# Kernel optimization log

Measured on AMD Instinct MI355X. Metric: run time of the kernel, lower is better.

The kernel has to match this reference:

```python
import jax, jax.numpy as jnp
import numpy as np

B, T, C, H = 2, 2048, 384, 6
HD = C // H
SINK_ITERS = 6  # MAX_ITER_SINK
EPS_LN = 1e-5


def layer_norm(x, w, b):
    mu = jnp.mean(x, axis=-1, keepdims=True)
    var = jnp.var(x, axis=-1, keepdims=True)
    return (x - mu) * jax.lax.rsqrt(var + EPS_LN) * w + b


def sinkhorn(c):
    # Log-domain Sinkhorn (sinkformers SinkhornDistance, eps=1, uniform 1/T marginals).
    # c: (B,H,T,T) row-softmaxed attention. C_cost=-c so M(C,u,v)= c + u_i + v_j.
    logT = jnp.log(jnp.asarray(T, c.dtype))
    u = jnp.zeros(c.shape[:-1], c.dtype)  # (B,H,T)
    v = jnp.zeros(c.shape[:-1], c.dtype)
    for i in range(SINK_ITERS):
        if i % 2 == 0:
            u = u - logT - jax.nn.logsumexp(c + u[..., :, None] + v[..., None, :], axis=-1)
        else:
            v = v - logT - jax.nn.logsumexp(c + u[..., :, None] + v[..., None, :], axis=-2)
            v = jax.lax.stop_gradient(v)  # torch code detaches v each odd iter
    return jnp.exp(c + u[..., :, None] + v[..., None, :])


def setup_inputs() -> dict:
    key = jax.random.key(0)
    ks = jax.random.split(key, 8)
    s = 0.02
    return {
        "x": jax.random.normal(ks[0], (B, T, C), jnp.float32),
        "t": jax.random.uniform(ks[1], (1,), jnp.float32),
        "ln1_w": jnp.ones((C + 1,), jnp.float32),
        "ln1_b": jnp.zeros((C + 1,), jnp.float32),
        "attn_w": (jax.random.normal(ks[2], (C + 1, 3 * C), jnp.float32) * s),  # torch W.T
        "attn_b": jnp.zeros((3 * C,), jnp.float32),
        "proj_w": (jax.random.normal(ks[3], (C, C), jnp.float32) * s),
        "proj_b": jnp.zeros((C,), jnp.float32),
        "ln2_w": jnp.ones((C + 1,), jnp.float32),
        "ln2_b": jnp.zeros((C + 1,), jnp.float32),
        "fc_w": (jax.random.normal(ks[4], (C + 1, 4 * C), jnp.float32) * s),
        "fc_b": jnp.zeros((4 * C,), jnp.float32),
        "fc2_w": (jax.random.normal(ks[5], (4 * C, C), jnp.float32) * s),
        "fc2_b": jnp.zeros((C,), jnp.float32),
    }


def add_time(h, t):
    b, tt, _ = h.shape
    tcol = jnp.broadcast_to(t.reshape(1, 1, 1).astype(h.dtype), (b, tt, 1))
    return jnp.concatenate([h, tcol], axis=-1)


def reference(x, t, ln1_w, ln1_b, attn_w, attn_b, proj_w, proj_b,
              ln2_w, ln2_b, fc_w, fc_b, fc2_w, fc2_b):
    # ---- attention sub-block ----
    xt = add_time(x, t)                       # (B,T,C+1)
    xn = layer_norm(xt, ln1_w, ln1_b)
    qkv = xn @ attn_w + attn_b                # (B,T,3C)
    q, k, vv = jnp.split(qkv, 3, axis=-1)
    q = q.reshape(B, T, H, HD).transpose(0, 2, 1, 3)   # (B,H,T,HD)
    k = k.reshape(B, T, H, HD).transpose(0, 2, 1, 3)
    vv = vv.reshape(B, T, H, HD).transpose(0, 2, 1, 3)
    att = jnp.einsum('bhqd,bhkd->bhqk', q, k) * (1.0 / np.sqrt(HD))
    causal = jnp.tril(jnp.ones((T, T), bool))
    att = jnp.where(causal, att, -jnp.inf)
    att = jax.nn.softmax(att, axis=-1)
    pi = sinkhorn(att) * T                    # sinked_att * last-dim size
    y = jnp.einsum('bhqk,bhkd->bhqd', pi, vv)
    y = y.transpose(0, 2, 1, 3).reshape(B, T, C)
    h = y @ proj_w + proj_b                   # (B,T,C)
    # ---- MLP sub-block ----
    ht = add_time(h, t)
    hn = layer_norm(ht, ln2_w, ln2_b)
    m = jax.nn.gelu(hn @ fc_w + fc_b, approximate=False)
    o = m @ fc2_w + fc2_b
    return o
```

## Files before the change

kernel.cpp:

```cpp
#include <hip/hip_runtime.h>
#include <hip/hip_fp16.h>
#include <math.h>

#define B 2
#define T 2048
#define C 384
#define H 6
#define HD 64
#define BHT (B*H*T)
#define LOGT 7.6246189861593985f

typedef __half half_t;
typedef _Float16 f16x8 __attribute__((ext_vector_type(8)));
typedef float f32x4 __attribute__((ext_vector_type(4)));

__device__ __forceinline__ float block_reduce_sum(float v) {
    __shared__ float sm[4];
    int lane = threadIdx.x & 63, wid = threadIdx.x >> 6;
#pragma unroll
    for (int o = 32; o > 0; o >>= 1) v += __shfl_down(v, o, 64);
    __syncthreads();
    if (lane == 0) sm[wid] = v;
    __syncthreads();
    return sm[0] + sm[1] + sm[2] + sm[3];
}

__device__ __forceinline__ float wave_allreduce_sum(float v) {
#pragma unroll
    for (int o = 1; o < 64; o <<= 1) v += __shfl_xor(v, o, 64);
    return v;
}

__global__ __launch_bounds__(256) void zerof_kernel(float* __restrict__ p) {
    p[(size_t)blockIdx.x * 256 + threadIdx.x] = 0.f;
}

__global__ __launch_bounds__(256) void addtime_ln_f16(
        const float* __restrict__ src, const float* __restrict__ tptr,
        const float* __restrict__ w, const float* __restrict__ bb,
        _Float16* __restrict__ dst, int KP) {
    const int n = C + 1;
    int row = blockIdx.x;
    const float* srow = src + (size_t)row * C;
    float tval = tptr[0];
    int i0 = threadIdx.x;
    int i1 = threadIdx.x + 256;
    float v0 = srow[i0];
    bool has1 = (i1 < n);
    float v1 = 0.f;
    if (has1) v1 = (i1 < C) ? srow[i1] : tval;
    float s  = block_reduce_sum(v0 + v1);
    float sq = block_reduce_sum(v0*v0 + v1*v1);
    float mean = s / n;
    float var  = sq / n - mean * mean;
    float rstd = rsqrtf(var + 1e-5f);
    _Float16* drow = dst + (size_t)row * KP;
    drow[i0] = (_Float16)((v0 - mean) * rstd * w[i0] + bb[i0]);
    if (has1) drow[i1] = (_Float16)((v1 - mean) * rstd * w[i1] + bb[i1]);
    else if (i1 < KP) drow[i1] = (_Float16)0.f;
}

__global__ __launch_bounds__(256) void convtrans_kernel(const float* __restrict__ W,
        _Float16* __restrict__ Wt, int K, int N, int KP) {
    __shared__ float tile[32][33];
    int k0 = blockIdx.x * 32, n0 = blockIdx.y * 32;
    int tx = threadIdx.x & 31, ty = threadIdx.x >> 5;
#pragma unroll
    for (int i = 0; i < 4; ++i) {
        int k = k0 + ty + i * 8, n = n0 + tx;
        tile[ty + i * 8][tx] = (k < K && n < N) ? W[(size_t)k * N + n] : 0.f;
    }
    __syncthreads();
#pragma unroll
    for (int i = 0; i < 4; ++i) {
        int n = n0 + ty + i * 8, k = k0 + tx;
        if (n < N && k < KP) Wt[(size_t)n * KP + k] = (_Float16)tile[tx][ty + i * 8];
    }
}

__device__ __forceinline__ f16x8 load8(const _Float16* p) { return *(const f16x8*)p; }
__device__ __forceinline__ f16x8 load8(const float* p) {
    float4 a = *(const float4*)p, b2 = *(const float4*)(p + 4);
    f16x8 r;
    r[0]=(_Float16)a.x; r[1]=(_Float16)a.y; r[2]=(_Float16)a.z; r[3]=(_Float16)a.w;
    r[4]=(_Float16)b2.x; r[5]=(_Float16)b2.y; r[6]=(_Float16)b2.z; r[7]=(_Float16)b2.w;
    return r;
}

template<int ACT, int QKV, typename AT, typename OUT_T>
__global__ __launch_bounds__(256) void mfma_gemm(
        const AT* __restrict__ A, const _Float16* __restrict__ Wt,
        const float* __restrict__ bias, OUT_T* __restrict__ out,
        int M, int N, int KP) {
    __shared__ __align__(16) _Float16 As[64][40];
    __shared__ __align__(16) _Float16 Bs[64][40];
    int tid = threadIdx.x;
    int lane = tid & 63, wave = tid >> 6;
    int wr = wave >> 1, wc = wave & 1;
    int m0 = blockIdx.y * 64, n0 = blockIdx.x * 64;
    int arow = tid >> 2, seg = tid & 3;
    int lrow = lane & 15, lseg = lane >> 4;
    f32x4 acc[2][2] = {};
    for (int k0 = 0; k0 < KP; k0 += 32) {
        __syncthreads();
        *(f16x8*)&As[arow][seg * 8] = load8(&A[(size_t)(m0 + arow) * KP + k0 + seg * 8]);
        *(f16x8*)&Bs[arow][seg * 8] = *(const f16x8*)&Wt[(size_t)(n0 + arow) * KP + k0 + seg * 8];
        __syncthreads();
        f16x8 af[2], bf[2];
#pragma unroll
        for (int i = 0; i < 2; ++i) af[i] = *(const f16x8*)&As[wr*32 + i*16 + lrow][lseg*8];
#pragma unroll
        for (int j = 0; j < 2; ++j) bf[j] = *(const f16x8*)&Bs[wc*32 + j*16 + lrow][lseg*8];
#pragma unroll
        for (int i = 0; i < 2; ++i)
#pragma unroll
            for (int j = 0; j < 2; ++j)
                acc[i][j] = __builtin_amdgcn_mfma_f32_16x16x32_f16(af[i], bf[j], acc[i][j], 0, 0, 0);
    }
    int lcol = lane & 15, lr4 = (lane >> 4) * 4;
#pragma unroll
    for (int i = 0; i < 2; ++i)
#pragma unroll
        for (int j = 0; j < 2; ++j) {
            int col = n0 + wc * 32 + j * 16 + lcol;
            float bv = bias[col];
#pragma unroll
            for (int r = 0; r < 4; ++r) {
                int row = m0 + wr * 32 + i * 16 + lr4 + r;
                float v = acc[i][j][r] + bv;
                if (ACT == 1) v = 0.5f * v * (1.f + erff(v * 0.70710678118654752f));
                if (QKV) {
                    int wq = col / C;
                    int rem = col - wq * C;
                    int hh = rem >> 6, dd = rem & 63;
                    int bb2 = row >> 11, tt = row & 2047;
                    out[(((size_t)wq * (B*H) + bb2 * H + hh) * T + tt) * 64 + dd] = (OUT_T)v;
                } else {
                    out[(size_t)row * N + col] = (OUT_T)v;
                }
            }
        }
}

__global__ __launch_bounds__(256) void qk_tileA(const _Float16* __restrict__ qh,
        const _Float16* __restrict__ kh, half_t* __restrict__ c_h) {
    int p = blockIdx.x, bh = blockIdx.y;
    int qt = (int)((sqrtf(8.f * (float)p + 1.f) - 1.f) * 0.5f);
    while ((qt + 1) * (qt + 2) / 2 <= p) ++qt;
    while (qt * (qt + 1) / 2 > p) --qt;
    int jt = p - qt * (qt + 1) / 2;
    int tid = threadIdx.x, lane = tid & 63, wave = tid >> 6;
    int wr = wave >> 1, wc = wave & 1;
    int lrow = lane & 15, lseg = lane >> 4;
    int orow = (lane >> 4) * 4, ocol = lane & 15;
    __shared__ __align__(16) _Float16 Qs[64][72];
    __shared__ __align__(16) _Float16 Ks[64][72];
    const _Float16* qb = qh + ((size_t)bh * T + qt * 64) * 64;
    const _Float16* kb = kh + ((size_t)bh * T + jt * 64) * 64;
#pragma unroll
    for (int k = 0; k < 2; ++k) {
        int cc = k * 256 + tid;
        int r = cc >> 3, sg = cc & 7;
        *(f16x8*)&Qs[r][sg*8] = *(const f16x8*)&qb[r*64 + sg*8];
        *(f16x8*)&Ks[r][sg*8] = *(const f16x8*)&kb[r*64 + sg*8];
    }
    __syncthreads();
    f32x4 acc[2][2] = {};
    f16x8 af[2], bf[2];
#pragma unroll
    for (int i = 0; i < 2; ++i) af[i] = *(const f16x8*)&Qs[wr*32+i*16+lrow][lseg*8];
#pragma unroll
    for (int j = 0; j < 2; ++j) bf[j] = *(const f16x8*)&Ks[wc*32+j*16+lrow][lseg*8];
#pragma unroll
    for (int i = 0; i < 2; ++i)
#pragma unroll
        for (int j = 0; j < 2; ++j)
            acc[i][j] = __builtin_amdgcn_mfma_f32_16x16x32_f16(af[i], bf[j], acc[i][j], 0,0,0);
#pragma unroll
    for (int i = 0; i < 2; ++i) af[i] = *(const f16x8*)&Qs[wr*32+i*16+lrow][32+lseg*8];
#pragma unroll
    for (int j = 0; j < 2; ++j) bf[j] = *(const f16x8*)&Ks[wc*32+j*16+lrow][32+lseg*8];
#pragma unroll
    for (int i = 0; i < 2; ++i)
#pragma unroll
        for (int j = 0; j < 2; ++j)
            acc[i][j] = __builtin_amdgcn_mfma_f32_16x16x32_f16(af[i], bf[j], acc[i][j], 0,0,0);
    __syncthreads();
    bool diag = (qt == jt);
#pragma unroll
    for (int i = 0; i < 2; ++i)
#pragma unroll
        for (int r = 0; r < 4; ++r) {
            int rl = wr*32 + i*16 + orow + r;
#pragma unroll
            for (int j = 0; j < 2; ++j) {
                int cl = wc*32 + j*16 + ocol;
                float s = acc[i][j][r] * 0.125f;
                float e = (diag && cl > rl) ? 0.f : __expf(s);
                Ks[rl][cl] = (_Float16)e;
            }
        }
    __syncthreads();
    half_t* cb = c_h + ((size_t)bh * T + qt * 64) * T + jt * 64;
#pragma unroll
    for (int k = 0; k < 2; ++k) {
        int cc = k * 256 + tid;
        int r = cc >> 3, sg = cc & 7;
        *(uint4*)&cb[(size_t)r * T + sg*8] = *(const uint4*)&Ks[r][sg*8];
    }
}

__global__ __launch_bounds__(256) void norm_q_u0(half_t* __restrict__ c_h,
        float* __restrict__ eu) {
    int tid = threadIdx.x, lane = tid & 63, wid = tid >> 6;
    int row = blockIdx.x * 4 + wid;
    int bh = row >> 11, i = row & 2047;
    int qt = i >> 6, span = (qt + 1) * 64, nch = span >> 3;
    half_t* crow = c_h + ((size_t)bh * T + i) * T;
    uint4 raw[4];
    float z = 0.f;
#pragma unroll
    for (int k = 0; k < 4; ++k) {
        int ch = lane + k * 64;
        if (ch < nch) {
            uint4 rw = *(const uint4*)(crow + ch * 8);
            raw[k] = rw;
            const __half2* h2 = (const __half2*)&rw;
#pragma unroll
            for (int pp = 0; pp < 4; ++pp) {
                float2 cf = __half22float2(h2[pp]);
                z += cf.x + cf.y;
            }
        }
    }
    z = wave_allreduce_sum(z);
    float inv = 1.f / z;
    float S = 0.f;
#pragma unroll
    for (int k = 0; k < 4; ++k) {
        int ch = lane + k * 64;
        if (ch < nch) {
            uint4 rw = raw[k];
            const __half2* h2 = (const __half2*)&rw;
            union { __half2 h2o[4]; uint4 u4; } ou;
#pragma unroll
            for (int pp = 0; pp < 4; ++pp) {
                float2 cf = __half22float2(h2[pp]);
                float q0 = __expf(cf.x * inv), q1 = __expf(cf.y * inv);
                S += q0 + q1;
                ou.h2o[pp] = __floats2half2_rn(q0, q1);
            }
            *(uint4*)(crow + ch * 8) = ou.u4;
        }
    }
    S = wave_allreduce_sum(S);
    if (lane == 0) eu[row] = 1.f / (2048.f * (S + (float)(T - span)));
}

template<int SUFFIX>
__global__ __launch_bounds__(256) void scan_sum_kernel(const float* __restrict__ src,
        float* __restrict__ dst) {
    int bh = blockIdx.x;
    int tid = threadIdx.x;
    __shared__ float part[256];
    __shared__ float ts[32];
    const float* s = src + (size_t)bh * T;
    float a = 0.f;
#pragma unroll
    for (int e = 0; e < 8; ++e) a += s[tid*8 + e];
    part[tid] = a;
    __syncthreads();
    if (tid < 32) {
        float t0 = 0.f;
#pragma unroll
        for (int k = 0; k < 8; ++k) t0 += part[tid*8 + k];
        ts[tid] = t0;
    }
    __syncthreads();
    if (tid == 0) {
        if (SUFFIX) {
            float run = 0.f;
            dst[bh*33 + 32] = 0.f;
            for (int kt = 31; kt >= 0; --kt) { run += ts[kt]; dst[bh*33+kt] = run; }
        } else {
            float run = 0.f;
            for (int kt = 0; kt < 33; ++kt) { dst[bh*33+kt] = run; if (kt < 32) run += ts[kt]; }
        }
    }
}

__global__ __launch_bounds__(256) void col_accum_mult(const half_t* __restrict__ c,
        const float* __restrict__ eu, float* __restrict__ acc) {
    int jb = blockIdx.x * 256;
    int r0 = blockIdx.y * 128;
    int bh = blockIdx.z;
    if (r0 + 128 <= jb) return;
    int tid = threadIdx.x;
    int j = jb + tid;
    int rstart = r0, wtile = jb + (tid & ~63);
    if (wtile > rstart) rstart = wtile;
    int rend = r0 + 128;
    const half_t* cb = c + (size_t)bh * T * T + j;
    const float* eub = eu + (size_t)bh * T;
    float a = 0.f;
#pragma unroll 8
    for (int r = rstart; r < rend; ++r)
        a = fmaf(__half2float(cb[(size_t)r * T]), eub[r], a);
    if (rstart < rend) atomicAdd(&acc[(size_t)bh * T + j], a);
}

__global__ __launch_bounds__(256) void v_finalize_mult(const float* __restrict__ acc,
        const float* __restrict__ peu, float* __restrict__ ev) {
    int idx = blockIdx.x * 256 + threadIdx.x;
    int bh = idx >> 11, j = idx & 2047;
    ev[idx] = 1.f / (2048.f * (acc[idx] + peu[bh*33 + (j >> 6)]));
}

__global__ __launch_bounds__(256) void row_eu_mult(const half_t* __restrict__ c,
        const float* __restrict__ ev, const float* __restrict__ sev,
        float* __restrict__ eu) {
    int tid = threadIdx.x, lane = tid & 63, wid = tid >> 6;
    int row = blockIdx.x * 4 + wid;
    int bh = row >> 11, i = row & 2047;
    int qt = i >> 6, nch = ((qt + 1) << 6) >> 3;
    const half_t* crow = c + ((size_t)bh * T + i) * T;
    const float* evb = ev + (size_t)bh * T;
    float s = 0.f;
#pragma unroll
    for (int k = 0; k < 4; ++k) {
        int ch = lane + k * 64;
        if (ch < nch) {
            uint4 rw = *(const uint4*)(crow + ch * 8);
            const __half2* h2 = (const __half2*)&rw;
            float4 e0 = *(const float4*)(evb + ch * 8);
            float4 e1 = *(const float4*)(evb + ch * 8 + 4);
            float2 c0 = __half22float2(h2[0]), c1 = __half22float2(h2[1]);
            float2 c2 = __half22float2(h2[2]), c3 = __half22float2(h2[3]);
            s = fmaf(c0.x, e0.x, s); s = fmaf(c0.y, e0.y, s);
            s = fmaf(c1.x, e0.z, s); s = fmaf(c1.y, e0.w, s);
            s = fmaf(c2.x, e1.x, s); s = fmaf(c2.y, e1.y, s);
            s = fmaf(c3.x, e1.z, s); s = fmaf(c3.y, e1.w, s);
        }
    }
    s = wave_allreduce_sum(s);
    if (lane == 0) eu[row] = 1.f / (2048.f * (s + sev[bh*33 + qt + 1]));
}

__global__ __launch_bounds__(256) void wv_suffix_kernel(const _Float16* __restrict__ vh,
        const float* __restrict__ ev, float* __restrict__ wsuf) {
    int bh = blockIdx.x;
    int tid = threadIdx.x;
    int d = tid & 63, g = tid >> 6;
    __shared__ float evs[2048];
    __shared__ float W[32][64];
    __shared__ float red[4][64];
    const float* vb = ev + (size_t)bh * T;
#pragma unroll
    for (int k = 0; k < 8; ++k) evs[tid + k*256] = vb[tid + k*256];
    __syncthreads();
    const _Float16* vbase = vh + (size_t)bh * T * 64;
    for (int jt = 0; jt < 32; ++jt) {
        float a = 0.f;
#pragma unroll
        for (int jj = 0; jj < 16; ++jj) {
            int j = jt*64 + g*16 + jj;
            a += evs[j] * (float)vbase[(size_t)j * 64 + d];
        }
        red[g][d] = a;
        __syncthreads();
        if (g == 0) W[jt][d] = red[0][d] + red[1][d] + red[2][d] + red[3][d];
        __syncthreads();
    }
    if (tid < 64) {
        float run = 0.f;
        wsuf[((size_t)bh*33 + 32)*64 + tid] = 0.f;
        for (int kt = 31; kt >= 0; --kt) {
            run += W[kt][tid];
            wsuf[((size_t)bh*33 + kt)*64 + tid] = run;
        }
    }
}

__global__ __launch_bounds__(256) void pv_split(const half_t* __restrict__ c_h,
        const float* __restrict__ eu, const float* __restrict__ ev,
        const _Float16* __restrict__ vh, const float* __restrict__ wsuf,
        float* __restrict__ y32) {
    int qt = blockIdx.x, kc = blockIdx.y, bh = blockIdx.z;
    int j0 = kc * 8;
    if (j0 > qt) return;
    int jend = min(qt + 1, j0 + 8);
    int b = bh / H, h = bh - b * H;
    int tid = threadIdx.x, lane = tid & 63, wave = tid >> 6;
    int wr = wave >> 1, wc = wave & 1;
    int lrow = lane & 15, lseg = lane >> 4;
    int orow = (lane >> 4) * 4, ocol = lane & 15;
    __shared__ __align__(16) _Float16 Ps[64][72];
    __shared__ __align__(16) _Float16 Vt[64][72];
    __shared__ float facs[64], vs[64], wsf[64];
    if (tid < 64) {
        facs[tid] = eu[(size_t)bh*T + qt*64 + tid] * 2048.f;
        if (kc == 0) wsf[tid] = wsuf[((size_t)bh*33 + qt + 1)*64 + tid];
    }
    f32x4 acc[2][2] = {};
    const half_t* cb0 = c_h + ((size_t)bh*T + qt*64)*T;
    for (int jt = j0; jt < jend; ++jt) {
        __syncthreads();
        if (tid < 64) vs[tid] = ev[(size_t)bh*T + jt*64 + tid];
        __syncthreads();
#pragma unroll
        for (int k = 0; k < 2; ++k) {
            int cc = k*256 + tid;
            int r = cc >> 3, sg = cc & 7;
            uint4 rw = *(const uint4*)&cb0[(size_t)r*T + jt*64 + sg*8];
            const __half2* h2 = (const __half2*)&rw;
            float fr = facs[r];
            f16x8 p8;
#pragma unroll
            for (int pp = 0; pp < 4; ++pp) {
                float2 cf = __half22float2(h2[pp]);
                p8[pp*2]   = (_Float16)(cf.x * fr * vs[sg*8 + pp*2]);
                p8[pp*2+1] = (_Float16)(cf.y * fr * vs[sg*8 + pp*2 + 1]);
            }
            *(f16x8*)&Ps[r][sg*8] = p8;
        }
        {
            const _Float16* vb = vh + ((size_t)bh*T + jt*64)*64;
#pragma unroll
            for (int k = 0; k < 2; ++k) {
                int d8 = (wave*2 + k) * 8;
                f16x8 v8 = *(const f16x8*)&vb[(size_t)lane*64 + d8];
#pragma unroll
                for (int e = 0; e < 8; ++e) Vt[d8 + e][lane] = v8[e];
            }
        }
        __syncthreads();
        f16x8 af[2], bf[2];
#pragma unroll
        for (int i = 0; i < 2; ++i) af[i] = *(const f16x8*)&Ps[wr*32+i*16+lrow][lseg*8];
#pragma unroll
        for (int j = 0; j < 2; ++j) bf[j] = *(const f16x8*)&Vt[wc*32+j*16+lrow][lseg*8];
#pragma unroll
        for (int i = 0; i < 2; ++i)
#pragma unroll
            for (int j = 0; j < 2; ++j)
                acc[i][j] = __builtin_amdgcn_mfma_f32_16x16x32_f16(af[i], bf[j], acc[i][j], 0,0,0);
#pragma unroll
        for (int i = 0; i < 2; ++i) af[i] = *(const f16x8*)&Ps[wr*32+i*16+lrow][32+lseg*8];
#pragma unroll
        for (int j = 0; j < 2; ++j) bf[j] = *(const f16x8*)&Vt[wc*32+j*16+lrow][32+lseg*8];
#pragma unroll
        for (int i = 0; i < 2; ++i)
#pragma unroll
            for (int j = 0; j < 2; ++j)
                acc[i][j] = __builtin_amdgcn_mfma_f32_16x16x32_f16(af[i], bf[j], acc[i][j], 0,0,0);
    }
#pragma unroll
    for (int i = 0; i < 2; ++i)
#pragma unroll
        for (int j = 0; j < 2; ++j)
#pragma unroll
            for (int r = 0; r < 4; ++r) {
                int rl = wr*32 + i*16 + orow + r;
                int cl = wc*32 + j*16 + ocol;
                float val = acc[i][j][r];
                if (kc == 0) val += facs[rl] * wsf[cl];
                atomicAdd(&y32[((size_t)b*T + qt*64 + rl)*C + h*HD + cl], val);
            }
}

extern "C" void kernel_launch(void* const* d_in, const int* in_sizes, int n_in,
                              void* d_out, int out_size, void* d_ws, size_t ws_size,
                              hipStream_t stream) {
    (void)in_sizes; (void)n_in; (void)out_size;
    const float* x      = (const float*)d_in[0];
    const float* t      = (const float*)d_in[1];
    const float* ln1_w  = (const float*)d_in[2];
    const float* ln1_b  = (const float*)d_in[3];
    const float* attn_w = (const float*)d_in[4];
    const float* attn_b = (const float*)d_in[5];
    const float* proj_w = (const float*)d_in[6];
    const float* proj_b = (const float*)d_in[7];
    const float* ln2_w  = (const float*)d_in[8];
    const float* ln2_b  = (const float*)d_in[9];
    const float* fc_w   = (const float*)d_in[10];
    const float* fc_b   = (const float*)d_in[11];
    const float* fc2_w  = (const float*)d_in[12];
    const float* fc2_b  = (const float*)d_in[13];
    float* out = (float*)d_out;

    if (ws_size < 121482240ull) return;
    char* wsb = (char*)d_ws;
    half_t*    c_h  = (half_t*)wsb;
    _Float16*  qkvh = (_Float16*)(wsb + 100663296ull);
    float*     y32  = (float*)(wsb + 110100480ull);
    _Float16*  xh   = (_Float16*)(wsb + 116391936ull);
    _Float16*  wbuf = (_Float16*)(wsb + 119799808ull);
    float*     eu   = (float*)(wsb + 121077760ull);
    float*     ev   = eu   + BHT;
    float*     cacc = ev   + BHT;
    float*     peu  = cacc + BHT;
    float*     sev  = peu  + 1024;
    float*     wsuf = sev  + 1024;
    const _Float16* qh = qkvh;
    const _Float16* kh = qkvh + (size_t)(B*H) * T * 64;
    const _Float16* vh = qkvh + (size_t)2 * (B*H) * T * 64;
    _Float16* xn_h = xh;
    _Float16* hn_h = xh;
    float*    hb   = (float*)qkvh;
    _Float16* mb_h = (_Float16*)wsb;

    const int M = B * T;
    const int KP1 = 416;

    addtime_ln_f16<<<M, 256, 0, stream>>>(x, t, ln1_w, ln1_b, xn_h, KP1);
    convtrans_kernel<<<dim3(KP1/32, (3*C)/32), 256, 0, stream>>>(attn_w, wbuf, C+1, 3*C, KP1);
    mfma_gemm<0, 1, _Float16, _Float16><<<dim3(3*C/64, M/64), 256, 0, stream>>>(
        xn_h, wbuf, attn_b, qkvh, M, 3*C, KP1);
    qk_tileA<<<dim3(528, B*H), 256, 0, stream>>>(qh, kh, c_h);
    norm_q_u0<<<BHT/4, 256, 0, stream>>>(c_h, eu);

    scan_sum_kernel<0><<<B*H, 256, 0, stream>>>(eu, peu);
    for (int it = 0; it < 3; ++it) {
        zerof_kernel<<<BHT/256, 256, 0, stream>>>(cacc);
        col_accum_mult<<<dim3(T/256, T/128, B*H), 256, 0, stream>>>(c_h, eu, cacc);
        v_finalize_mult<<<BHT/256, 256, 0, stream>>>(cacc, peu, ev);
        if (it < 2) {
            scan_sum_kernel<1><<<B*H, 256, 0, stream>>>(ev, sev);
            row_eu_mult<<<BHT/4, 256, 0, stream>>>(c_h, ev, sev, eu);
            scan_sum_kernel<0><<<B*H, 256, 0, stream>>>(eu, peu);
        }
    }
    wv_suffix_kernel<<<B*H, 256, 0, stream>>>(vh, ev, wsuf);
    zerof_kernel<<<(M*C)/256, 256, 0, stream>>>(y32);
    pv_split<<<dim3(T/64, 4, B*H), 256, 0, stream>>>(c_h, eu, ev, vh, wsuf, y32);

    convtrans_kernel<<<dim3(C/32, C/32), 256, 0, stream>>>(proj_w, wbuf, C, C, C);
    mfma_gemm<0, 0, float, float><<<dim3(C/64, M/64), 256, 0, stream>>>(
        y32, wbuf, proj_b, hb, M, C, C);

    addtime_ln_f16<<<M, 256, 0, stream>>>(hb, t, ln2_w, ln2_b, hn_h, KP1);
    convtrans_kernel<<<dim3(KP1/32, (4*C)/32), 256, 0, stream>>>(fc_w, wbuf, C+1, 4*C, KP1);
    mfma_gemm<1, 0, _Float16, _Float16><<<dim3(4*C/64, M/64), 256, 0, stream>>>(
        hn_h, wbuf, fc_b, mb_h, M, 4*C, KP1);
    convtrans_kernel<<<dim3((4*C)/32, C/32), 256, 0, stream>>>(fc2_w, wbuf, 4*C, C, 4*C);
    mfma_gemm<0, 0, _Float16, float><<<dim3(C/64, M/64), 256, 0, stream>>>(
        mb_h, wbuf, fc2_b, out, M, C, 4*C);
}
```

Measured before the change: 348.3 us.

## Fuse Sinkhorn row and column passes into single sweeps over attention matrix

Merges the row-normalisation pass with the column accumulation, so each sweep over the fp16 attention matrix computes the row scaling and also accumulates the column sums for the next half-iteration, using per-wave register and shared-memory partials followed by atomics. The separate prefix and suffix scan, zeroing and finalize kernels are folded into one per-head kernel that also resets the accumulator. This roughly halves the passes over the large T×T matrix and removes several launches, at the cost of heavier register use, a 32 KB shared buffer per block and only 768 blocks with an uneven causal workload.

```diff
diff --git a/kernel.cpp b/kernel.cpp
--- a/kernel.cpp
+++ b/kernel.cpp
@@ -210,140 +210,207 @@
     }
 }
 
-__global__ __launch_bounds__(256) void norm_q_u0(half_t* __restrict__ c_h,
-        float* __restrict__ eu) {
-    int tid = threadIdx.x, lane = tid & 63, wid = tid >> 6;
-    int row = blockIdx.x * 4 + wid;
-    int bh = row >> 11, i = row & 2047;
-    int qt = i >> 6, span = (qt + 1) * 64, nch = span >> 3;
-    half_t* crow = c_h + ((size_t)bh * T + i) * T;
-    uint4 raw[4];
-    float z = 0.f;
+__global__ __launch_bounds__(256) void norm_q_col(half_t* __restrict__ c_h,
+        float* __restrict__ eu, float* __restrict__ cacc) {
+    int qt = blockIdx.x >> 1, half = blockIdx.x & 1, bh = blockIdx.y;
+    int tid = threadIdx.x, lane = tid & 63, w = tid >> 6;
+    int span = (qt + 1) * 64, nch = span >> 3;
+    __shared__ float colacc[4][2048];
+    float acc32[32];
+#pragma unroll
+    for (int k = 0; k < 32; ++k) acc32[k] = 0.f;
+    half_t* cb = c_h + ((size_t)bh * T + qt * 64 + half * 32) * T;
+    for (int rr = 0; rr < 8; ++rr) {
+        int i = w * 8 + rr;
+        half_t* crow = cb + (size_t)i * T;
+        uint4 raw[4];
+        float z = 0.f;
+#pragma unroll
+        for (int k = 0; k < 4; ++k) {
+            int ch = lane + (k << 6);
+            if (ch < nch) {
+                uint4 rw = *(const uint4*)(crow + ch * 8);
+                raw[k] = rw;
+                const __half2* h2 = (const __half2*)&rw;
+#pragma unroll
+                for (int pp = 0; pp < 4; ++pp) {
+                    float2 cf = __half22float2(h2[pp]);
+                    z += cf.x + cf.y;
+                }
+            }
+        }
+        z = wave_allreduce_sum(z);
+        float inv = 1.f / z;
+        float qv[32];
+        float S = 0.f;
+#pragma unroll
+        for (int k = 0; k < 4; ++k) {
+            int ch = lane + (k << 6);
+            if (ch < nch) {
+                const __half2* h2 = (const __half2*)&raw[k];
+                union { __half2 h[4]; uint4 u; } ou;
+#pragma unroll
+                for (int pp = 0; pp < 4; ++pp) {
+                    float2 cf = __half22float2(h2[pp]);
+                    float q0 = __expf(cf.x * inv), q1 = __expf(cf.y * inv);
+                    S += q0 + q1;
+                    qv[k*8+pp*2] = q0; qv[k*8+pp*2+1] = q1;
+                    ou.h[pp] = __floats2half2_rn(q0, q1);
+                }
+                *(uint4*)(crow + ch * 8) = ou.u;
+            }
+        }
+        S = wave_allreduce_sum(S);
+        float eui = 1.f / (2048.f * (S + (float)(T - span)));
+        if (lane == 0) eu[(size_t)bh * T + qt * 64 + half * 32 + i] = eui;
+#pragma unroll
+        for (int k = 0; k < 4; ++k) {
+            int ch = lane + (k << 6);
+            if (ch < nch)
+#pragma unroll
+                for (int e = 0; e < 8; ++e)
+                    acc32[k*8+e] = fmaf(qv[k*8+e], eui, acc32[k*8+e]);
+        }
+    }
 #pragma unroll
     for (int k = 0; k < 4; ++k) {
-        int ch = lane + k * 64;
+        int ch = lane + (k << 6);
+        if (ch < nch)
+#pragma unroll
+            for (int e = 0; e < 8; ++e)
+                colacc[w][ch*8+e] = acc32[k*8+e];
+    }
+    __syncthreads();
+    for (int j = tid; j < span; j += 256)
+        atomicAdd(&cacc[(size_t)bh*T + j],
+                  colacc[0][j]+colacc[1][j]+colacc[2][j]+colacc[3][j]);
+}
+
+__global__ __launch_bounds__(256) void row_col(const half_t* __restrict__ c_h,
+        const float* __restrict__ ev, const float* __restrict__ sev,
+        float* __restrict__ eu, float* __restrict__ cacc) {
+    int qt = blockIdx.x >> 1, half = blockIdx.x & 1, bh = blockIdx.y;
+    int tid = threadIdx.x, lane = tid & 63, w = tid >> 6;
+    int span = (qt + 1) * 64, nch = span >> 3;
+    __shared__ float colacc[4][2048];
+    float evreg[32], acc32[32];
+#pragma unroll
+    for (int k = 0; k < 32; ++k) acc32[k] = 0.f;
+    const float* evb = ev + (size_t)bh * T;
+#pragma unroll
+    for (int k = 0; k < 4; ++k) {
+        int ch = lane + (k << 6);
         if (ch < nch) {
-            uint4 rw = *(const uint4*)(crow + ch * 8);
-            raw[k] = rw;
-            const __half2* h2 = (const __half2*)&rw;
-#pragma unroll
-            for (int pp = 0; pp < 4; ++pp) {
-                float2 cf = __half22float2(h2[pp]);
-                z += cf.x + cf.y;
-            }
-        }
-    }
-    z = wave_allreduce_sum(z);
-    float inv = 1.f / z;
-    float S = 0.f;
+            float4 e0 = *(const float4*)(evb + ch*8);
+            float4 e1 = *(const float4*)(evb + ch*8 + 4);
+            evreg[k*8+0]=e0.x; evreg[k*8+1]=e0.y; evreg[k*8+2]=e0.z; evreg[k*8+3]=e0.w;
+            evreg[k*8+4]=e1.x; evreg[k*8+5]=e1.y; evreg[k*8+6]=e1.z; evreg[k*8+7]=e1.w;
+        }
+    }
+    float tail = sev[bh*33 + qt + 1];
+    const half_t* cb = c_h + ((size_t)bh * T + qt * 64 + half * 32) * T;
+    for (int rr = 0; rr < 8; ++rr) {
+        int i = w * 8 + rr;
+        const half_t* crow = cb + (size_t)i * T;
+        uint4 raw[4];
+        float s = 0.f;
+#pragma unroll
+        for (int k = 0; k < 4; ++k) {
+            int ch = lane + (k << 6);
+            if (ch < nch) {
+                uint4 rw = *(const uint4*)(crow + ch * 8);
+                raw[k] = rw;
+                const __half2* h2 = (const __half2*)&rw;
+#pragma unroll
+                for (int pp = 0; pp < 4; ++pp) {
+                    float2 cf = __half22float2(h2[pp]);
+                    s = fmaf(cf.x, evreg[k*8+pp*2],   s);
+                    s = fmaf(cf.y, evreg[k*8+pp*2+1], s);
+                }
+            }
+        }
+        s = wave_allreduce_sum(s);
+        float eui = 1.f / (2048.f * (s + tail));
+        if (lane == 0) eu[(size_t)bh * T + qt * 64 + half * 32 + i] = eui;
+#pragma unroll
+        for (int k = 0; k < 4; ++k) {
+            int ch = lane + (k << 6);
+            if (ch < nch) {
+                const __half2* h2 = (const __half2*)&raw[k];
+#pragma unroll
+                for (int pp = 0; pp < 4; ++pp) {
+                    float2 cf = __half22float2(h2[pp]);
+                    acc32[k*8+pp*2]   = fmaf(cf.x, eui, acc32[k*8+pp*2]);
+                    acc32[k*8+pp*2+1] = fmaf(cf.y, eui, acc32[k*8+pp*2+1]);
+                }
+            }
+        }
+    }
 #pragma unroll
     for (int k = 0; k < 4; ++k) {
-        int ch = lane + k * 64;
-        if (ch < nch) {
-            uint4 rw = raw[k];
-            const __half2* h2 = (const __half2*)&rw;
-            union { __half2 h2o[4]; uint4 u4; } ou;
-#pragma unroll
-            for (int pp = 0; pp < 4; ++pp) {
-                float2 cf = __half22float2(h2[pp]);
-                float q0 = __expf(cf.x * inv), q1 = __expf(cf.y * inv);
-                S += q0 + q1;
-                ou.h2o[pp] = __floats2half2_rn(q0, q1);
-            }
-            *(uint4*)(crow + ch * 8) = ou.u4;
-        }
-    }
-    S = wave_allreduce_sum(S);
-    if (lane == 0) eu[row] = 1.f / (2048.f * (S + (float)(T - span)));
-}
-
-template<int SUFFIX>
-__global__ __launch_bounds__(256) void scan_sum_kernel(const float* __restrict__ src,
-        float* __restrict__ dst) {
+        int ch = lane + (k << 6);
+        if (ch < nch)
+#pragma unroll
+            for (int e = 0; e < 8; ++e)
+                colacc[w][ch*8+e] = acc32[k*8+e];
+    }
+    __syncthreads();
+    for (int j = tid; j < span; j += 256)
+        atomicAdd(&cacc[(size_t)bh*T + j],
+                  colacc[0][j]+colacc[1][j]+colacc[2][j]+colacc[3][j]);
+}
+
+__global__ __launch_bounds__(256) void v_fin_full(float* __restrict__ cacc,
+        const float* __restrict__ eu, float* __restrict__ ev,
+        float* __restrict__ sev) {
     int bh = blockIdx.x;
     int tid = threadIdx.x;
     __shared__ float part[256];
-    __shared__ float ts[32];
-    const float* s = src + (size_t)bh * T;
+    __shared__ float pre[33];
+    __shared__ float ts2[32];
+    const float* eub = eu + (size_t)bh * T;
+    float* caccb = cacc + (size_t)bh * T;
+    float* evb = ev + (size_t)bh * T;
     float a = 0.f;
 #pragma unroll
-    for (int e = 0; e < 8; ++e) a += s[tid*8 + e];
+    for (int e = 0; e < 8; ++e) a += eub[tid*8 + e];
     part[tid] = a;
+    __syncthreads();
+    if (tid == 0) {
+        float run = 0.f;
+        for (int kt = 0; kt < 32; ++kt) {
+            pre[kt] = run;
+            float t0 = 0.f;
+            for (int k = 0; k < 8; ++k) t0 += part[kt*8 + k];
+            run += t0;
+        }
+        pre[32] = run;
+    }
+    __syncthreads();
+    float p = pre[tid >> 3];
+    float b2 = 0.f;
+#pragma unroll
+    for (int e = 0; e < 8; ++e) {
+        int j = tid*8 + e;
+        float vj = 1.f / (2048.f * (caccb[j] + p));
+        evb[j] = vj;
+        caccb[j] = 0.f;
+        b2 += vj;
+    }
+    part[tid] = b2;
     __syncthreads();
     if (tid < 32) {
         float t0 = 0.f;
 #pragma unroll
         for (int k = 0; k < 8; ++k) t0 += part[tid*8 + k];
-        ts[tid] = t0;
+        ts2[tid] = t0;
     }
     __syncthreads();
     if (tid == 0) {
-        if (SUFFIX) {
-            float run = 0.f;
-            dst[bh*33 + 32] = 0.f;
-            for (int kt = 31; kt >= 0; --kt) { run += ts[kt]; dst[bh*33+kt] = run; }
-        } else {
-            float run = 0.f;
-            for (int kt = 0; kt < 33; ++kt) { dst[bh*33+kt] = run; if (kt < 32) run += ts[kt]; }
-        }
-    }
-}
-
-__global__ __launch_bounds__(256) void col_accum_mult(const half_t* __restrict__ c,
-        const float* __restrict__ eu, float* __restrict__ acc) {
-    int jb = blockIdx.x * 256;
-    int r0 = blockIdx.y * 128;
-    int bh = blockIdx.z;
-    if (r0 + 128 <= jb) return;
-    int tid = threadIdx.x;
-    int j = jb + tid;
-    int rstart = r0, wtile = jb + (tid & ~63);
-    if (wtile > rstart) rstart = wtile;
-    int rend = r0 + 128;
-    const half_t* cb = c + (size_t)bh * T * T + j;
-    const float* eub = eu + (size_t)bh * T;
-    float a = 0.f;
-#pragma unroll 8
-    for (int r = rstart; r < rend; ++r)
-        a = fmaf(__half2float(cb[(size_t)r * T]), eub[r], a);
-    if (rstart < rend) atomicAdd(&acc[(size_t)bh * T + j], a);
-}
-
-__global__ __launch_bounds__(256) void v_finalize_mult(const float* __restrict__ acc,
-        const float* __restrict__ peu, float* __restrict__ ev) {
-    int idx = blockIdx.x * 256 + threadIdx.x;
-    int bh = idx >> 11, j = idx & 2047;
-    ev[idx] = 1.f / (2048.f * (acc[idx] + peu[bh*33 + (j >> 6)]));
-}
-
-__global__ __launch_bounds__(256) void row_eu_mult(const half_t* __restrict__ c,
-        const float* __restrict__ ev, const float* __restrict__ sev,
-        float* __restrict__ eu) {
-    int tid = threadIdx.x, lane = tid & 63, wid = tid >> 6;
-    int row = blockIdx.x * 4 + wid;
-    int bh = row >> 11, i = row & 2047;
-    int qt = i >> 6, nch = ((qt + 1) << 6) >> 3;
-    const half_t* crow = c + ((size_t)bh * T + i) * T;
-    const float* evb = ev + (size_t)bh * T;
-    float s = 0.f;
-#pragma unroll
-    for (int k = 0; k < 4; ++k) {
-        int ch = lane + k * 64;
-        if (ch < nch) {
-            uint4 rw = *(const uint4*)(crow + ch * 8);
-            const __half2* h2 = (const __half2*)&rw;
-            float4 e0 = *(const float4*)(evb + ch * 8);
-            float4 e1 = *(const float4*)(evb + ch * 8 + 4);
-            float2 c0 = __half22float2(h2[0]), c1 = __half22float2(h2[1]);
-            float2 c2 = __half22float2(h2[2]), c3 = __half22float2(h2[3]);
-            s = fmaf(c0.x, e0.x, s); s = fmaf(c0.y, e0.y, s);
-            s = fmaf(c1.x, e0.z, s); s = fmaf(c1.y, e0.w, s);
-            s = fmaf(c2.x, e1.x, s); s = fmaf(c2.y, e1.y, s);
-            s = fmaf(c3.x, e1.z, s); s = fmaf(c3.y, e1.w, s);
-        }
-    }
-    s = wave_allreduce_sum(s);
-    if (lane == 0) eu[row] = 1.f / (2048.f * (s + sev[bh*33 + qt + 1]));
+        float run = 0.f;
+        sev[bh*33 + 32] = 0.f;
+        for (int kt = 31; kt >= 0; --kt) { run += ts2[kt]; sev[bh*33 + kt] = run; }
+    }
 }
 
 __global__ __launch_bounds__(256) void wv_suffix_kernel(const _Float16* __restrict__ vh,
@@ -498,8 +565,7 @@
     float*     eu   = (float*)(wsb + 121077760ull);
     float*     ev   = eu   + BHT;
     float*     cacc = ev   + BHT;
-    float*     peu  = cacc + BHT;
-    float*     sev  = peu  + 1024;
+    float*     sev  = cacc + BHT;
     float*     wsuf = sev  + 1024;
     const _Float16* qh = qkvh;
     const _Float16* kh = qkvh + (size_t)(B*H) * T * 64;
@@ -517,19 +583,15 @@
     mfma_gemm<0, 1, _Float16, _Float16><<<dim3(3*C/64, M/64), 256, 0, stream>>>(
         xn_h, wbuf, attn_b, qkvh, M, 3*C, KP1);
     qk_tileA<<<dim3(528, B*H), 256, 0, stream>>>(qh, kh, c_h);
-    norm_q_u0<<<BHT/4, 256, 0, stream>>>(c_h, eu);
-
-    scan_sum_kernel<0><<<B*H, 256, 0, stream>>>(eu, peu);
-    for (int it = 0; it < 3; ++it) {
-        zerof_kernel<<<BHT/256, 256, 0, stream>>>(cacc);
-        col_accum_mult<<<dim3(T/256, T/128, B*H), 256, 0, stream>>>(c_h, eu, cacc);
-        v_finalize_mult<<<BHT/256, 256, 0, stream>>>(cacc, peu, ev);
-        if (it < 2) {
-            scan_sum_kernel<1><<<B*H, 256, 0, stream>>>(ev, sev);
-            row_eu_mult<<<BHT/4, 256, 0, stream>>>(c_h, ev, sev, eu);
-            scan_sum_kernel<0><<<B*H, 256, 0, stream>>>(eu, peu);
-        }
-    }
+
+    zerof_kernel<<<BHT/256, 256, 0, stream>>>(cacc);
+    norm_q_col<<<dim3(64, B*H), 256, 0, stream>>>(c_h, eu, cacc);
+    v_fin_full<<<B*H, 256, 0, stream>>>(cacc, eu, ev, sev);
+    row_col<<<dim3(64, B*H), 256, 0, stream>>>(c_h, ev, sev, eu, cacc);
+    v_fin_full<<<B*H, 256, 0, stream>>>(cacc, eu, ev, sev);
+    row_col<<<dim3(64, B*H), 256, 0, stream>>>(c_h, ev, sev, eu, cacc);
+    v_fin_full<<<B*H, 256, 0, stream>>>(cacc, eu, ev, sev);
+
     wv_suffix_kernel<<<B*H, 256, 0, stream>>>(vh, ev, wsuf);
     zerof_kernel<<<(M*C)/256, 256, 0, stream>>>(y32);
     pv_split<<<dim3(T/64, 4, B*H), 256, 0, stream>>>(c_h, eu, ev, vh, wsuf, y32);
```

After: 321.6 us. -7.7%, faster.
